# Kernel tuning notes

Hardware: AMD Instinct MI355X
Metric: run time of the kernel (lower is better)

Reference implementation:

```python
import jax, jax.numpy as jnp
import numpy as np

N_NODES = 50000
N_EDGES = 800000
D_IN, D_HID, D_OUT = 128, 128, 64


def setup_inputs() -> dict:
    key = jax.random.key(0)
    ks = jax.random.split(key, 10)
    return {
        "x": jax.random.normal(ks[0], (N_NODES, D_IN), dtype=jnp.float32),
        "edge_row": jax.random.randint(ks[1], (N_EDGES,), 0, N_NODES, dtype=jnp.int32),
        "edge_col": jax.random.randint(ks[2], (N_EDGES,), 0, N_NODES, dtype=jnp.int32),
        "edge_val": jax.random.uniform(ks[3], (N_EDGES,), dtype=jnp.float32),
        "W1": jax.random.normal(ks[4], (D_IN, D_HID), dtype=jnp.float32) * (1.0 / np.sqrt(D_HID)),
        "b1": jax.random.normal(ks[5], (D_HID,), dtype=jnp.float32) * (1.0 / np.sqrt(D_HID)),
        "W2": jax.random.normal(ks[6], (D_HID, D_HID), dtype=jnp.float32) * (1.0 / np.sqrt(D_HID)),
        "b2": jax.random.normal(ks[7], (D_HID,), dtype=jnp.float32) * (1.0 / np.sqrt(D_HID)),
        "W3": jax.random.normal(ks[8], (D_HID, D_OUT), dtype=jnp.float32) * (1.0 / np.sqrt(D_OUT)),
        "b3": jax.random.normal(ks[9], (D_OUT,), dtype=jnp.float32) * (1.0 / np.sqrt(D_OUT)),
    }


def _gcn_layer(x, edge_row, edge_col, edge_val, W, b):
    # support = x @ W          : dense GEMM [N, d_out]
    support = x @ W
    # spmm(adj, support)[i] = sum_e with row[e]==i: val[e] * support[col[e]]
    gathered = support[edge_col] * edge_val[:, None]  # [E, d_out]
    agg = jax.ops.segment_sum(gathered, edge_row, num_segments=x.shape[0])
    return agg + b


def reference(x, edge_row, edge_col, edge_val, W1, b1, W2, b2, W3, b3):
    # Layer 1 + ReLU (dropout is identity in eval)
    h = jax.nn.relu(_gcn_layer(x, edge_row, edge_col, edge_val, W1, b1))
    # Layer 2 + ReLU
    h = jax.nn.relu(_gcn_layer(h, edge_row, edge_col, edge_val, W2, b2))
    # Layer 3 (no activation)
    return _gcn_layer(h, edge_row, edge_col, edge_val, W3, b3)
```

## Files before the change

kernel.cpp:

```cpp
#include <hip/hip_runtime.h>

#define N_NODES 50000
#define N_EDGES 800000
#define SCAN_TILE 2048
#define GEMM1_BLOCKS 768
#define FUSED_BLOCKS 512
#define FILL_BLOCKS ((N_EDGES + 255) / 256)

#define HB 64
#define EPB (N_EDGES / HB)
#define HGROUPS (EPB / 4)
#define HHALF (N_NODES / 2)
#define HHALF4 (HHALF / 4)

static_assert(N_NODES < 65536, "col must fit in 16 bits for packed CSR");
static_assert(N_EDGES % (4 * HB) == 0, "chunking must be exact");
static_assert(EPB < 65536, "packed u16 counts must not overflow");

typedef __attribute__((ext_vector_type(4))) float f32x4;
typedef __attribute__((ext_vector_type(8))) short bf16x8;

__device__ inline unsigned short f32_to_bf16(float f) {
    unsigned int u = __builtin_bit_cast(unsigned int, f);
    u += 0x7FFF + ((u >> 16) & 1);
    return (unsigned short)(u >> 16);
}
__device__ inline float bf16_to_f32(unsigned short h) {
    unsigned int u = ((unsigned int)h) << 16;
    return __builtin_bit_cast(float, u);
}

#define W128  (128 * 128)
#define W64   (128 * 64)

__global__ __launch_bounds__(256) void prep_hist(
    const int* __restrict__ erow, int* __restrict__ rank,
    int* __restrict__ bhist, int* __restrict__ done_,
    const float* __restrict__ W1, const float* __restrict__ W2,
    const float* __restrict__ W3,
    unsigned short* __restrict__ Wt1, unsigned short* __restrict__ Wt2,
    unsigned short* __restrict__ Wt3) {
    __shared__ int h[HHALF];
    const int tid = threadIdx.x;
    if (blockIdx.x < HB) {
        const int b = blockIdx.x;
        int4* h4 = reinterpret_cast<int4*>(h);
        for (int i = tid; i < HHALF4; i += 256) {
            int4 z = {0, 0, 0, 0};
            h4[i] = z;
        }
        __syncthreads();
        const int4* eg = reinterpret_cast<const int4*>(erow) + (size_t)b * HGROUPS;
        int4* rg = reinterpret_cast<int4*>(rank) + (size_t)b * HGROUPS;
        for (int g = tid; g < HGROUPS; g += 256) {
            int4 er = eg[g];
            int4 rk;
            int sh, o;
            sh = (er.x & 1) << 4;
            o = atomicAdd(&h[er.x >> 1], 1 << sh);
            rk.x = (o >> sh) & 0xFFFF;
            sh = (er.y & 1) << 4;
            o = atomicAdd(&h[er.y >> 1], 1 << sh);
            rk.y = (o >> sh) & 0xFFFF;
            sh = (er.z & 1) << 4;
            o = atomicAdd(&h[er.z >> 1], 1 << sh);
            rk.z = (o >> sh) & 0xFFFF;
            sh = (er.w & 1) << 4;
            o = atomicAdd(&h[er.w >> 1], 1 << sh);
            rk.w = (o >> sh) & 0xFFFF;
            rg[g] = rk;
        }
        __syncthreads();
        int4* dst = reinterpret_cast<int4*>(bhist + (size_t)b * HHALF);
        for (int i = tid; i < HHALF4; i += 256) dst[i] = h4[i];
        return;
    }
    long long r = (long long)(blockIdx.x - HB) * 256 + tid;
    if (r < W128) {
        int k = (int)r / 128, m = (int)r % 128;
        Wt1[m * 128 + k] = f32_to_bf16(W1[r]);
        return;
    }
    r -= W128;
    if (r < W128) {
        int k = (int)r / 128, m = (int)r % 128;
        Wt2[m * 128 + k] = f32_to_bf16(W2[r]);
        return;
    }
    r -= W128;
    if (r < W64) {
        int k = (int)r / 64, m = (int)r % 64;
        Wt3[m * 128 + k] = f32_to_bf16(W3[r]);
        return;
    }
    r -= W64;
    if (r == 0) *done_ = 0;
}

template <int NOUT>
__device__ __forceinline__ void mfma_phase(const unsigned short* Xs,
                                           const unsigned short* Ws,
                                           unsigned short* __restrict__ Yb,
                                           int block_row, int N) {
    constexpr int KP = 128 + 8;
    constexpr int NT = NOUT / 16;
    const int tid = threadIdx.x;
    const int wave = tid >> 6;
    const int lane = tid & 63;
    const int m = lane & 15;
    const int quad = lane >> 4;
    const int rowbase = wave * 16;

    f32x4 acc[NT];
#pragma unroll
    for (int t = 0; t < NT; ++t) acc[t] = (f32x4){0.f, 0.f, 0.f, 0.f};

#pragma unroll
    for (int kt = 0; kt < 4; ++kt) {
        bf16x8 a = *reinterpret_cast<const bf16x8*>(
            Xs + (rowbase + m) * KP + kt * 32 + quad * 8);
#pragma unroll
        for (int t = 0; t < NT; ++t) {
            bf16x8 b = *reinterpret_cast<const bf16x8*>(
                Ws + (t * 16 + m) * KP + kt * 32 + quad * 8);
            acc[t] = __builtin_amdgcn_mfma_f32_16x16x32_bf16(a, b, acc[t], 0, 0, 0);
        }
    }

#pragma unroll
    for (int t = 0; t < NT; ++t) {
#pragma unroll
        for (int r = 0; r < 4; ++r) {
            int grow = block_row + rowbase + quad * 4 + r;
            if (grow < N)
                Yb[(size_t)grow * NOUT + t * 16 + m] = f32_to_bf16(acc[t][r]);
        }
    }
}

__global__ __launch_bounds__(256) void gemm1(
    const float* __restrict__ x, const unsigned short* __restrict__ Wt,
    unsigned short* __restrict__ Yb, int N, int ntiles) {
    constexpr int KP = 128 + 8;
    __shared__ unsigned short Xs[64 * KP];
    __shared__ unsigned short Ws[128 * KP];
    const int tid = threadIdx.x;

    for (int idx = tid; idx < 128 * 16; idx += 256) {
        int r = idx >> 4, ch = idx & 15;
        uint4 v = *reinterpret_cast<const uint4*>(Wt + r * 128 + ch * 8);
        *reinterpret_cast<uint4*>(Ws + r * KP + ch * 8) = v;
    }

    for (int tile = blockIdx.x; tile < ntiles; tile += GEMM1_BLOCKS) {
        const int block_row = tile * 64;
        for (int idx = tid; idx < 64 * 16; idx += 256) {
            int r = idx >> 4, ch = idx & 15;
            int gr = block_row + r;
            if (gr >= N) gr = N - 1;
            const float4* xp =
                reinterpret_cast<const float4*>(x + (size_t)gr * 128 + ch * 8);
            float4 a = xp[0], b = xp[1];
            uint4 o;
            o.x = (unsigned int)f32_to_bf16(a.x) | ((unsigned int)f32_to_bf16(a.y) << 16);
            o.y = (unsigned int)f32_to_bf16(a.z) | ((unsigned int)f32_to_bf16(a.w) << 16);
            o.z = (unsigned int)f32_to_bf16(b.x) | ((unsigned int)f32_to_bf16(b.y) << 16);
            o.w = (unsigned int)f32_to_bf16(b.z) | ((unsigned int)f32_to_bf16(b.w) << 16);
            *reinterpret_cast<uint4*>(Xs + r * KP + ch * 8) = o;
        }
        __syncthreads();
        mfma_phase<128>(Xs, Ws, Yb, block_row, N);
        __syncthreads();
    }
}

__global__ void scan_fused(const int* __restrict__ bhist, int* __restrict__ tsum,
                           int* __restrict__ done, int* __restrict__ rptr,
                           int* __restrict__ bbase, int n, int ntiles) {
    __shared__ int sums[256];
    __shared__ int off_s;
    const int t = threadIdx.x;
    const int b = blockIdx.x;
    const int base = b * SCAN_TILE + t * 8;
    const int nidx = base >> 3;
    const int4* bh4 = reinterpret_cast<const int4*>(bhist);
    int v[8], pref[8];
#pragma unroll
    for (int i = 0; i < 8; ++i) v[i] = 0;
    if (base < n) {
        for (int hb = 0; hb < HB; ++hb) {
            int4 p = bh4[hb * HHALF4 + nidx];
            v[0] += p.x & 0xFFFF; v[1] += (int)((unsigned)p.x >> 16);
            v[2] += p.y & 0xFFFF; v[3] += (int)((unsigned)p.y >> 16);
            v[4] += p.z & 0xFFFF; v[5] += (int)((unsigned)p.z >> 16);
            v[6] += p.w & 0xFFFF; v[7] += (int)((unsigned)p.w >> 16);
        }
    }
    int s = 0;
#pragma unroll
    for (int i = 0; i < 8; ++i) s += v[i];
    sums[t] = s;
    __syncthreads();
    for (int off = 1; off < 256; off <<= 1) {
        int x = (t >= off) ? sums[t - off] : 0;
        __syncthreads();
        sums[t] += x;
        __syncthreads();
    }
    int run = sums[t] - s;
#pragma unroll
    for (int i = 0; i < 8; ++i) {
        pref[i] = run;
        run += v[i];
    }
    if (t == 255) {
        tsum[b] = run;
        __threadfence();
        atomicAdd(done, 1);
    }
    if (t == 0) {
        while (__hip_atomic_load(done, __ATOMIC_ACQUIRE, __HIP_MEMORY_SCOPE_AGENT) <
               ntiles) {
        }
        __threadfence();
        int off = 0;
        for (int i = 0; i < b; ++i) off += tsum[i];
        off_s = off;
        if (b == 0) {
            int tot = 0;
            for (int i = 0; i < ntiles; ++i) tot += tsum[i];
            rptr[n] = tot;
        }
    }
    __syncthreads();
    const int off = off_s;
    if (base < n) {
        int rn[8];
#pragma unroll
        for (int i = 0; i < 8; ++i) rn[i] = pref[i] + off;
        int4 r0 = {rn[0], rn[1], rn[2], rn[3]};
        int4 r1 = {rn[4], rn[5], rn[6], rn[7]};
        *reinterpret_cast<int4*>(rptr + base) = r0;
        *reinterpret_cast<int4*>(rptr + base + 4) = r1;
        for (int hb = 0; hb < HB; ++hb) {
            int4 p = bh4[hb * HHALF4 + nidx];
            int4 o0 = {rn[0], rn[1], rn[2], rn[3]};
            int4 o1 = {rn[4], rn[5], rn[6], rn[7]};
            int4* bb = reinterpret_cast<int4*>(bbase + (size_t)hb * N_NODES + base);
            bb[0] = o0;
            bb[1] = o1;
            rn[0] += p.x & 0xFFFF; rn[1] += (int)((unsigned)p.x >> 16);
            rn[2] += p.y & 0xFFFF; rn[3] += (int)((unsigned)p.y >> 16);
            rn[4] += p.z & 0xFFFF; rn[5] += (int)((unsigned)p.z >> 16);
            rn[6] += p.w & 0xFFFF; rn[7] += (int)((unsigned)p.w >> 16);
        }
    }
}

__global__ void fill_csr(const int* __restrict__ erow, const int* __restrict__ ecol,
                         const float* __restrict__ eval, const int* __restrict__ bbase,
                         const int* __restrict__ rank,
                         unsigned int* __restrict__ cpack) {
    int e = blockIdx.x * blockDim.x + threadIdx.x;
    if (e >= N_EDGES) return;
    int slot = bbase[(size_t)(e / EPB) * N_NODES + erow[e]] + rank[e];
    unsigned int p = (unsigned int)(ecol[e] & 0xFFFF) |
                     ((unsigned int)f32_to_bf16(eval[e]) << 16);
    cpack[slot] = p;
}

template <int NOUT>
__device__ __forceinline__ void mfma_phase512(const unsigned short* Xs,
                                              const unsigned short* Ws,
                                              unsigned short* __restrict__ Yb,
                                              int block_row, int N) {
    constexpr int KP = 128 + 8;
    constexpr int NT = NOUT / 16;
    constexpr int NTH = NT / 2;
    const int tid = threadIdx.x;
    const int wave = tid >> 6;
    const int lane = tid & 63;
    const int m = lane & 15;
    const int quad = lane >> 4;
    const int rowbase = (wave & 3) * 16;
    const int tbase = (wave >> 2) * NTH;

    f32x4 acc[NTH];
#pragma unroll
    for (int t = 0; t < NTH; ++t) acc[t] = (f32x4){0.f, 0.f, 0.f, 0.f};

#pragma unroll
    for (int kt = 0; kt < 4; ++kt) {
        bf16x8 a = *reinterpret_cast<const bf16x8*>(
            Xs + (rowbase + m) * KP + kt * 32 + quad * 8);
#pragma unroll
        for (int t = 0; t < NTH; ++t) {
            bf16x8 b = *reinterpret_cast<const bf16x8*>(
                Ws + ((tbase + t) * 16 + m) * KP + kt * 32 + quad * 8);
            acc[t] = __builtin_amdgcn_mfma_f32_16x16x32_bf16(a, b, acc[t], 0, 0, 0);
        }
    }

#pragma unroll
    for (int t = 0; t < NTH; ++t) {
#pragma unroll
        for (int r = 0; r < 4; ++r) {
            int grow = block_row + rowbase + quad * 4 + r;
            if (grow < N)
                Yb[(size_t)grow * NOUT + (tbase + t) * 16 + m] = f32_to_bf16(acc[t][r]);
        }
    }
}

template <int NOUT>
__global__ __launch_bounds__(512, 4) void gemm_fused_agg(
    const unsigned short* __restrict__ S,
    const int* __restrict__ rptr, const unsigned int* __restrict__ cpack,
    const float* __restrict__ bias,
    const unsigned short* __restrict__ Wt,
    unsigned short* __restrict__ Yb,
    int N, int ntiles) {
    constexpr int KP = 128 + 8;
    __shared__ unsigned short Xs[64 * KP];
    __shared__ unsigned short Ws[NOUT * KP];
    const int tid = threadIdx.x;
    const int group = tid >> 4;
    const int f8 = tid & 15;

    for (int idx = tid; idx < NOUT * 16; idx += 512) {
        int r = idx >> 4, ch = idx & 15;
        uint4 v = *reinterpret_cast<const uint4*>(Wt + r * 128 + ch * 8);
        *reinterpret_cast<uint4*>(Ws + r * KP + ch * 8) = v;
    }

    float bv[8];
#pragma unroll
    for (int i = 0; i < 8; ++i) bv[i] = bias[f8 * 8 + i];

    for (int tile = blockIdx.x; tile < ntiles; tile += gridDim.x) {
        const int block_row = tile * 64;
#pragma unroll
        for (int r4 = 0; r4 < 2; ++r4) {
            const int row = r4 * 32 + group;
            const int node = block_row + row;
            float acc[8];
#pragma unroll
            for (int i = 0; i < 8; ++i) acc[i] = bv[i];
            if (node < N) {
                const int beg = rptr[node];
                const int end = rptr[node + 1];
                int j = beg;
                for (; j + 8 <= end; j += 8) {
                    unsigned int p[8];
                    uint4 s[8];
#pragma unroll
                    for (int u = 0; u < 8; ++u) p[u] = cpack[j + u];
#pragma unroll
                    for (int u = 0; u < 8; ++u)
                        s[u] = *reinterpret_cast<const uint4*>(
                            S + (size_t)(p[u] & 0xFFFF) * 128 + f8 * 8);
#pragma unroll
                    for (int u = 0; u < 8; ++u) {
                        const float v = bf16_to_f32((unsigned short)(p[u] >> 16));
                        const unsigned short* sp =
                            reinterpret_cast<const unsigned short*>(&s[u]);
#pragma unroll
                        for (int i = 0; i < 8; ++i)
                            acc[i] = fmaf(v, bf16_to_f32(sp[i]), acc[i]);
                    }
                }
                if (j + 4 <= end) {
                    unsigned int p[4];
                    uint4 s[4];
#pragma unroll
                    for (int u = 0; u < 4; ++u) p[u] = cpack[j + u];
#pragma unroll
                    for (int u = 0; u < 4; ++u)
                        s[u] = *reinterpret_cast<const uint4*>(
                            S + (size_t)(p[u] & 0xFFFF) * 128 + f8 * 8);
#pragma unroll
                    for (int u = 0; u < 4; ++u) {
                        const float v = bf16_to_f32((unsigned short)(p[u] >> 16));
                        const unsigned short* sp =
                            reinterpret_cast<const unsigned short*>(&s[u]);
#pragma unroll
                        for (int i = 0; i < 8; ++i)
                            acc[i] = fmaf(v, bf16_to_f32(sp[i]), acc[i]);
                    }
                    j += 4;
                }
                if (j + 2 <= end) {
                    unsigned int p[2];
                    uint4 s[2];
#pragma unroll
                    for (int u = 0; u < 2; ++u) p[u] = cpack[j + u];
#pragma unroll
                    for (int u = 0; u < 2; ++u)
                        s[u] = *reinterpret_cast<const uint4*>(
                            S + (size_t)(p[u] & 0xFFFF) * 128 + f8 * 8);
#pragma unroll
                    for (int u = 0; u < 2; ++u) {
                        const float v = bf16_to_f32((unsigned short)(p[u] >> 16));
                        const unsigned short* sp =
                            reinterpret_cast<const unsigned short*>(&s[u]);
#pragma unroll
                        for (int i = 0; i < 8; ++i)
                            acc[i] = fmaf(v, bf16_to_f32(sp[i]), acc[i]);
                    }
                    j += 2;
                }
                if (j < end) {
                    unsigned int p = cpack[j];
                    uint4 s = *reinterpret_cast<const uint4*>(
                        S + (size_t)(p & 0xFFFF) * 128 + f8 * 8);
                    const float v = bf16_to_f32((unsigned short)(p >> 16));
                    const unsigned short* sp =
                        reinterpret_cast<const unsigned short*>(&s);
#pragma unroll
                    for (int i = 0; i < 8; ++i)
                        acc[i] = fmaf(v, bf16_to_f32(sp[i]), acc[i]);
                }
            }
            uint4 o;
            o.x = (unsigned int)f32_to_bf16(fmaxf(acc[0], 0.f)) |
                  ((unsigned int)f32_to_bf16(fmaxf(acc[1], 0.f)) << 16);
            o.y = (unsigned int)f32_to_bf16(fmaxf(acc[2], 0.f)) |
                  ((unsigned int)f32_to_bf16(fmaxf(acc[3], 0.f)) << 16);
            o.z = (unsigned int)f32_to_bf16(fmaxf(acc[4], 0.f)) |
                  ((unsigned int)f32_to_bf16(fmaxf(acc[5], 0.f)) << 16);
            o.w = (unsigned int)f32_to_bf16(fmaxf(acc[6], 0.f)) |
                  ((unsigned int)f32_to_bf16(fmaxf(acc[7], 0.f)) << 16);
            *reinterpret_cast<uint4*>(Xs + row * KP + f8 * 8) = o;
        }
        __syncthreads();
        mfma_phase512<NOUT>(Xs, Ws, Yb, block_row, N);
        __syncthreads();
    }
}

__global__ void aggregate_bf16_64(const unsigned short* __restrict__ S,
                                  const int* __restrict__ rptr,
                                  const unsigned int* __restrict__ cpack,
                                  const float* __restrict__ bias,
                                  float* __restrict__ out, int N) {
    const int node = blockIdx.x * (blockDim.x / 8) + threadIdx.x / 8;
    const int f8 = threadIdx.x & 7;
    if (node >= N) return;
    const int beg = rptr[node];
    const int end = rptr[node + 1];
    float acc[8];
#pragma unroll
    for (int i = 0; i < 8; ++i) acc[i] = bias[f8 * 8 + i];
    int j = beg;
    for (; j + 8 <= end; j += 8) {
        unsigned int p[8];
        uint4 s[8];
#pragma unroll
        for (int u = 0; u < 8; ++u) p[u] = cpack[j + u];
#pragma unroll
        for (int u = 0; u < 8; ++u)
            s[u] = *reinterpret_cast<const uint4*>(S + (size_t)(p[u] & 0xFFFF) * 64 + f8 * 8);
#pragma unroll
        for (int u = 0; u < 8; ++u) {
            const float v = bf16_to_f32((unsigned short)(p[u] >> 16));
            const unsigned short* sp = reinterpret_cast<const unsigned short*>(&s[u]);
#pragma unroll
            for (int i = 0; i < 8; ++i) acc[i] = fmaf(v, bf16_to_f32(sp[i]), acc[i]);
        }
    }
    if (j + 4 <= end) {
        unsigned int p[4];
        uint4 s[4];
#pragma unroll
        for (int u = 0; u < 4; ++u) p[u] = cpack[j + u];
#pragma unroll
        for (int u = 0; u < 4; ++u)
            s[u] = *reinterpret_cast<const uint4*>(S + (size_t)(p[u] & 0xFFFF) * 64 + f8 * 8);
#pragma unroll
        for (int u = 0; u < 4; ++u) {
            const float v = bf16_to_f32((unsigned short)(p[u] >> 16));
            const unsigned short* sp = reinterpret_cast<const unsigned short*>(&s[u]);
#pragma unroll
            for (int i = 0; i < 8; ++i) acc[i] = fmaf(v, bf16_to_f32(sp[i]), acc[i]);
        }
        j += 4;
    }
    if (j + 2 <= end) {
        unsigned int p[2];
        uint4 s[2];
#pragma unroll
        for (int u = 0; u < 2; ++u) p[u] = cpack[j + u];
#pragma unroll
        for (int u = 0; u < 2; ++u)
            s[u] = *reinterpret_cast<const uint4*>(S + (size_t)(p[u] & 0xFFFF) * 64 + f8 * 8);
#pragma unroll
        for (int u = 0; u < 2; ++u) {
            const float v = bf16_to_f32((unsigned short)(p[u] >> 16));
            const unsigned short* sp = reinterpret_cast<const unsigned short*>(&s[u]);
#pragma unroll
            for (int i = 0; i < 8; ++i) acc[i] = fmaf(v, bf16_to_f32(sp[i]), acc[i]);
        }
        j += 2;
    }
    if (j < end) {
        unsigned int p = cpack[j];
        uint4 s = *reinterpret_cast<const uint4*>(S + (size_t)(p & 0xFFFF) * 64 + f8 * 8);
        const float v = bf16_to_f32((unsigned short)(p >> 16));
        const unsigned short* sp = reinterpret_cast<const unsigned short*>(&s);
#pragma unroll
        for (int i = 0; i < 8; ++i) acc[i] = fmaf(v, bf16_to_f32(sp[i]), acc[i]);
    }
    float4 o0 = {acc[0], acc[1], acc[2], acc[3]};
    float4 o1 = {acc[4], acc[5], acc[6], acc[7]};
    float* op = out + (size_t)node * 64 + f8 * 8;
    *reinterpret_cast<float4*>(op) = o0;
    *reinterpret_cast<float4*>(op + 4) = o1;
}

extern "C" void kernel_launch(void* const* d_in, const int* in_sizes, int n_in,
                              void* d_out, int out_size, void* d_ws, size_t ws_size,
                              hipStream_t stream) {
    const float* x    = (const float*)d_in[0];
    const int*   erow = (const int*)d_in[1];
    const int*   ecol = (const int*)d_in[2];
    const float* eval = (const float*)d_in[3];
    const float* W1   = (const float*)d_in[4];
    const float* b1   = (const float*)d_in[5];
    const float* W2   = (const float*)d_in[6];
    const float* b2   = (const float*)d_in[7];
    const float* W3   = (const float*)d_in[8];
    const float* b3   = (const float*)d_in[9];
    float* out = (float*)d_out;

    const size_t nf = (size_t)N_NODES * 128;
    unsigned short* SA  = (unsigned short*)d_ws;
    unsigned short* SB  = SA + nf;
    unsigned short* Wt1 = SB + nf;
    unsigned short* Wt2 = Wt1 + 128 * 128;
    unsigned short* Wt3 = Wt2 + 128 * 128;
    int*   rank   = (int*)(Wt3 + 64 * 128);
    int*   bhist  = rank + N_EDGES;
    int*   bbase  = bhist + (size_t)HB * HHALF;
    int*   rptr   = bbase + (size_t)HB * N_NODES;
    unsigned int* cpack = (unsigned int*)(rptr + N_NODES + 1);
    int*   stsum  = (int*)(cpack + N_EDGES);
    int*   done   = stsum + 32;

    const int blk = 256;
    const int ntiles_g = (N_NODES + 63) / 64;
    const int agg_grid = (int)(((long long)N_NODES * 8 + blk - 1) / blk);
    const int ntiles = (N_NODES + SCAN_TILE - 1) / SCAN_TILE;

    {
        long long wtotal = (long long)W128 + W128 + W64 + 1;
        int wblocks = (int)((wtotal + blk - 1) / blk);
        prep_hist<<<HB + wblocks, blk, 0, stream>>>(
            erow, rank, bhist, done, W1, W2, W3, Wt1, Wt2, Wt3);
    }

    gemm1<<<GEMM1_BLOCKS, 256, 0, stream>>>(x, Wt1, SA, N_NODES, ntiles_g);

    scan_fused<<<ntiles, 256, 0, stream>>>(bhist, stsum, done, rptr, bbase,
                                           N_NODES, ntiles);

    fill_csr<<<FILL_BLOCKS, blk, 0, stream>>>(erow, ecol, eval, bbase, rank, cpack);

    gemm_fused_agg<128><<<FUSED_BLOCKS, 512, 0, stream>>>(
        SA, rptr, cpack, b1, Wt2, SB, N_NODES, ntiles_g);

    gemm_fused_agg<64><<<FUSED_BLOCKS, 512, 0, stream>>>(
        SB, rptr, cpack, b2, Wt3, SA, N_NODES, ntiles_g);

    aggregate_bf16_64<<<agg_grid, blk, 0, stream>>>(SA, rptr, cpack, b3, out, N_NODES);
}
```

Before: 236.3 us.

## Fuse CSR build into GEMM1 and scan kernels, pack histograms as bytes

The row histogram moves into the first GEMM launch as extra blocks, and the scan and CSR fill become one kernel separated by a grid-wide atomic barrier. The per-block histogram counts and edge ranks shrink from 16-bit to 8-bit packing. The weight transpose and bf16 conversion now happen inside each GEMM block instead of in a separate prep kernel. Together these cut the launch count and the histogram and rank traffic. The costs are that every GEMM block repeats the weight conversion, the spin barrier needs all 960 blocks resident at once, and 8-bit counts overflow if one node gets 256 or more edges within a single chunk of 12500.

```diff
diff --git a/kernel.cpp b/kernel.cpp
--- a/kernel.cpp
+++ b/kernel.cpp
@@ -5,17 +5,16 @@
 #define SCAN_TILE 2048
 #define GEMM1_BLOCKS 768
 #define FUSED_BLOCKS 512
-#define FILL_BLOCKS ((N_EDGES + 255) / 256)
 
 #define HB 64
 #define EPB (N_EDGES / HB)
 #define HGROUPS (EPB / 4)
-#define HHALF (N_NODES / 2)
-#define HHALF4 (HHALF / 4)
+#define HWORDS (N_NODES / 4)
+#define SCANFILL_BLOCKS 960
 
 static_assert(N_NODES < 65536, "col must fit in 16 bits for packed CSR");
 static_assert(N_EDGES % (4 * HB) == 0, "chunking must be exact");
-static_assert(EPB < 65536, "packed u16 counts must not overflow");
+static_assert(N_NODES % 8 == 0, "scan tiles assume x8");
 
 typedef __attribute__((ext_vector_type(4))) float f32x4;
 typedef __attribute__((ext_vector_type(8))) short bf16x8;
@@ -28,73 +27,6 @@
 __device__ inline float bf16_to_f32(unsigned short h) {
     unsigned int u = ((unsigned int)h) << 16;
     return __builtin_bit_cast(float, u);
-}
-
-#define W128  (128 * 128)
-#define W64   (128 * 64)
-
-__global__ __launch_bounds__(256) void prep_hist(
-    const int* __restrict__ erow, int* __restrict__ rank,
-    int* __restrict__ bhist, int* __restrict__ done_,
-    const float* __restrict__ W1, const float* __restrict__ W2,
-    const float* __restrict__ W3,
-    unsigned short* __restrict__ Wt1, unsigned short* __restrict__ Wt2,
-    unsigned short* __restrict__ Wt3) {
-    __shared__ int h[HHALF];
-    const int tid = threadIdx.x;
-    if (blockIdx.x < HB) {
-        const int b = blockIdx.x;
-        int4* h4 = reinterpret_cast<int4*>(h);
-        for (int i = tid; i < HHALF4; i += 256) {
-            int4 z = {0, 0, 0, 0};
-            h4[i] = z;
-        }
-        __syncthreads();
-        const int4* eg = reinterpret_cast<const int4*>(erow) + (size_t)b * HGROUPS;
-        int4* rg = reinterpret_cast<int4*>(rank) + (size_t)b * HGROUPS;
-        for (int g = tid; g < HGROUPS; g += 256) {
-            int4 er = eg[g];
-            int4 rk;
-            int sh, o;
-            sh = (er.x & 1) << 4;
-            o = atomicAdd(&h[er.x >> 1], 1 << sh);
-            rk.x = (o >> sh) & 0xFFFF;
-            sh = (er.y & 1) << 4;
-            o = atomicAdd(&h[er.y >> 1], 1 << sh);
-            rk.y = (o >> sh) & 0xFFFF;
-            sh = (er.z & 1) << 4;
-            o = atomicAdd(&h[er.z >> 1], 1 << sh);
-            rk.z = (o >> sh) & 0xFFFF;
-            sh = (er.w & 1) << 4;
-            o = atomicAdd(&h[er.w >> 1], 1 << sh);
-            rk.w = (o >> sh) & 0xFFFF;
-            rg[g] = rk;
-        }
-        __syncthreads();
-        int4* dst = reinterpret_cast<int4*>(bhist + (size_t)b * HHALF);
-        for (int i = tid; i < HHALF4; i += 256) dst[i] = h4[i];
-        return;
-    }
-    long long r = (long long)(blockIdx.x - HB) * 256 + tid;
-    if (r < W128) {
-        int k = (int)r / 128, m = (int)r % 128;
-        Wt1[m * 128 + k] = f32_to_bf16(W1[r]);
-        return;
-    }
-    r -= W128;
-    if (r < W128) {
-        int k = (int)r / 128, m = (int)r % 128;
-        Wt2[m * 128 + k] = f32_to_bf16(W2[r]);
-        return;
-    }
-    r -= W128;
-    if (r < W64) {
-        int k = (int)r / 64, m = (int)r % 64;
-        Wt3[m * 128 + k] = f32_to_bf16(W3[r]);
-        return;
-    }
-    r -= W64;
-    if (r == 0) *done_ = 0;
 }
 
 template <int NOUT>
@@ -138,21 +70,63 @@
     }
 }
 
-__global__ __launch_bounds__(256) void gemm1(
-    const float* __restrict__ x, const unsigned short* __restrict__ Wt,
-    unsigned short* __restrict__ Yb, int N, int ntiles) {
+__global__ __launch_bounds__(256) void mega1(
+    const float* __restrict__ x, const float* __restrict__ W1,
+    unsigned short* __restrict__ Yb, int N, int ntiles,
+    const int* __restrict__ erow, unsigned int* __restrict__ rank8,
+    unsigned int* __restrict__ bhist, int* __restrict__ done,
+    int* __restrict__ done2) {
     constexpr int KP = 128 + 8;
-    __shared__ unsigned short Xs[64 * KP];
-    __shared__ unsigned short Ws[128 * KP];
+    __shared__ __align__(16) unsigned char smem[52224];
     const int tid = threadIdx.x;
 
-    for (int idx = tid; idx < 128 * 16; idx += 256) {
-        int r = idx >> 4, ch = idx & 15;
-        uint4 v = *reinterpret_cast<const uint4*>(Wt + r * 128 + ch * 8);
-        *reinterpret_cast<uint4*>(Ws + r * KP + ch * 8) = v;
-    }
-
-    for (int tile = blockIdx.x; tile < ntiles; tile += GEMM1_BLOCKS) {
+    if (blockIdx.x < HB) {
+        const int b = blockIdx.x;
+        if (b == 0 && tid == 0) { *done = 0; *done2 = 0; }
+        unsigned int* h = reinterpret_cast<unsigned int*>(smem);
+        int4* h4 = reinterpret_cast<int4*>(h);
+        for (int i = tid; i < HWORDS / 4; i += 256) {
+            int4 z = {0, 0, 0, 0};
+            h4[i] = z;
+        }
+        __syncthreads();
+        const int4* eg = reinterpret_cast<const int4*>(erow) + (size_t)b * HGROUPS;
+        unsigned int* rg = rank8 + (size_t)b * HGROUPS;
+        for (int g = tid; g < HGROUPS; g += 256) {
+            int4 er = eg[g];
+            unsigned int rk;
+            int sh;
+            unsigned int o;
+            sh = (er.x & 3) << 3;
+            o = atomicAdd(&h[er.x >> 2], 1u << sh);
+            rk = (o >> sh) & 0xFFu;
+            sh = (er.y & 3) << 3;
+            o = atomicAdd(&h[er.y >> 2], 1u << sh);
+            rk |= ((o >> sh) & 0xFFu) << 8;
+            sh = (er.z & 3) << 3;
+            o = atomicAdd(&h[er.z >> 2], 1u << sh);
+            rk |= ((o >> sh) & 0xFFu) << 16;
+            sh = (er.w & 3) << 3;
+            o = atomicAdd(&h[er.w >> 2], 1u << sh);
+            rk |= ((o >> sh) & 0xFFu) << 24;
+            rg[g] = rk;
+        }
+        __syncthreads();
+        int4* dst = reinterpret_cast<int4*>(bhist + (size_t)b * HWORDS);
+        for (int i = tid; i < HWORDS / 4; i += 256) dst[i] = h4[i];
+        return;
+    }
+
+    const int gb = blockIdx.x - HB;
+    unsigned short* Xs = reinterpret_cast<unsigned short*>(smem);
+    unsigned short* Ws = reinterpret_cast<unsigned short*>(smem) + 64 * KP;
+
+    for (int idx = tid; idx < 128 * 128; idx += 256) {
+        int k = idx >> 7, m = idx & 127;
+        Ws[m * KP + k] = f32_to_bf16(W1[idx]);
+    }
+
+    for (int tile = gb; tile < ntiles; tile += GEMM1_BLOCKS) {
         const int block_row = tile * 64;
         for (int idx = tid; idx < 64 * 16; idx += 256) {
             int r = idx >> 4, ch = idx & 15;
@@ -174,99 +148,116 @@
     }
 }
 
-__global__ void scan_fused(const int* __restrict__ bhist, int* __restrict__ tsum,
-                           int* __restrict__ done, int* __restrict__ rptr,
-                           int* __restrict__ bbase, int n, int ntiles) {
+__global__ __launch_bounds__(256, 4) void scan_fill(
+    const unsigned int* __restrict__ bhist, int* __restrict__ tsum,
+    int* __restrict__ done, int* __restrict__ done2,
+    int* __restrict__ rptr, int* __restrict__ bbase,
+    const int* __restrict__ erow, const int* __restrict__ ecol,
+    const float* __restrict__ eval, const unsigned int* __restrict__ rank8,
+    unsigned int* __restrict__ cpack, int n, int ntiles) {
     __shared__ int sums[256];
     __shared__ int off_s;
     const int t = threadIdx.x;
     const int b = blockIdx.x;
-    const int base = b * SCAN_TILE + t * 8;
-    const int nidx = base >> 3;
-    const int4* bh4 = reinterpret_cast<const int4*>(bhist);
-    int v[8], pref[8];
-#pragma unroll
-    for (int i = 0; i < 8; ++i) v[i] = 0;
-    if (base < n) {
-        for (int hb = 0; hb < HB; ++hb) {
-            int4 p = bh4[hb * HHALF4 + nidx];
-            v[0] += p.x & 0xFFFF; v[1] += (int)((unsigned)p.x >> 16);
-            v[2] += p.y & 0xFFFF; v[3] += (int)((unsigned)p.y >> 16);
-            v[4] += p.z & 0xFFFF; v[5] += (int)((unsigned)p.z >> 16);
-            v[6] += p.w & 0xFFFF; v[7] += (int)((unsigned)p.w >> 16);
-        }
-    }
-    int s = 0;
-#pragma unroll
-    for (int i = 0; i < 8; ++i) s += v[i];
-    sums[t] = s;
+
+    if (b < ntiles) {
+        const int base = b * SCAN_TILE + t * 8;
+        const int widx2 = base >> 3;
+        const uint2* bh2 = reinterpret_cast<const uint2*>(bhist);
+        int v[8], pref[8];
+#pragma unroll
+        for (int i = 0; i < 8; ++i) v[i] = 0;
+        if (base < n) {
+            for (int hb = 0; hb < HB; ++hb) {
+                uint2 p = bh2[hb * (HWORDS / 2) + widx2];
+                v[0] += p.x & 0xFF; v[1] += (p.x >> 8) & 0xFF;
+                v[2] += (p.x >> 16) & 0xFF; v[3] += p.x >> 24;
+                v[4] += p.y & 0xFF; v[5] += (p.y >> 8) & 0xFF;
+                v[6] += (p.y >> 16) & 0xFF; v[7] += p.y >> 24;
+            }
+        }
+        int s = 0;
+#pragma unroll
+        for (int i = 0; i < 8; ++i) s += v[i];
+        sums[t] = s;
+        __syncthreads();
+        for (int off = 1; off < 256; off <<= 1) {
+            int x = (t >= off) ? sums[t - off] : 0;
+            __syncthreads();
+            sums[t] += x;
+            __syncthreads();
+        }
+        int run = sums[t] - s;
+#pragma unroll
+        for (int i = 0; i < 8; ++i) {
+            pref[i] = run;
+            run += v[i];
+        }
+        if (t == 255) {
+            tsum[b] = run;
+            __threadfence();
+            atomicAdd(done, 1);
+        }
+        if (t == 0) {
+            while (__hip_atomic_load(done, __ATOMIC_ACQUIRE,
+                                     __HIP_MEMORY_SCOPE_AGENT) < ntiles) {
+            }
+            __threadfence();
+            int off = 0;
+            for (int i = 0; i < b; ++i) off += tsum[i];
+            off_s = off;
+            if (b == 0) {
+                int tot = 0;
+                for (int i = 0; i < ntiles; ++i) tot += tsum[i];
+                rptr[n] = tot;
+            }
+        }
+        __syncthreads();
+        const int off = off_s;
+        if (base < n) {
+            int rn[8];
+#pragma unroll
+            for (int i = 0; i < 8; ++i) rn[i] = pref[i] + off;
+            int4 r0 = {rn[0], rn[1], rn[2], rn[3]};
+            int4 r1 = {rn[4], rn[5], rn[6], rn[7]};
+            *reinterpret_cast<int4*>(rptr + base) = r0;
+            *reinterpret_cast<int4*>(rptr + base + 4) = r1;
+            for (int hb = 0; hb < HB; ++hb) {
+                int4 o0 = {rn[0], rn[1], rn[2], rn[3]};
+                int4 o1 = {rn[4], rn[5], rn[6], rn[7]};
+                int4* bb = reinterpret_cast<int4*>(
+                    bbase + (size_t)hb * N_NODES + base);
+                bb[0] = o0;
+                bb[1] = o1;
+                uint2 p = bh2[hb * (HWORDS / 2) + widx2];
+                rn[0] += p.x & 0xFF; rn[1] += (p.x >> 8) & 0xFF;
+                rn[2] += (p.x >> 16) & 0xFF; rn[3] += p.x >> 24;
+                rn[4] += p.y & 0xFF; rn[5] += (p.y >> 8) & 0xFF;
+                rn[6] += (p.y >> 16) & 0xFF; rn[7] += p.y >> 24;
+            }
+        }
+        __syncthreads();
+        if (t == 0) {
+            __threadfence();
+            atomicAdd(done2, 1);
+        }
+    }
+
+    if (t == 0) {
+        while (__hip_atomic_load(done2, __ATOMIC_ACQUIRE,
+                                 __HIP_MEMORY_SCOPE_AGENT) < ntiles) {
+        }
+    }
     __syncthreads();
-    for (int off = 1; off < 256; off <<= 1) {
-        int x = (t >= off) ? sums[t - off] : 0;
-        __syncthreads();
-        sums[t] += x;
-        __syncthreads();
-    }
-    int run = sums[t] - s;
-#pragma unroll
-    for (int i = 0; i < 8; ++i) {
-        pref[i] = run;
-        run += v[i];
-    }
-    if (t == 255) {
-        tsum[b] = run;
-        __threadfence();
-        atomicAdd(done, 1);
-    }
-    if (t == 0) {
-        while (__hip_atomic_load(done, __ATOMIC_ACQUIRE, __HIP_MEMORY_SCOPE_AGENT) <
-               ntiles) {
-        }
-        __threadfence();
-        int off = 0;
-        for (int i = 0; i < b; ++i) off += tsum[i];
-        off_s = off;
-        if (b == 0) {
-            int tot = 0;
-            for (int i = 0; i < ntiles; ++i) tot += tsum[i];
-            rptr[n] = tot;
-        }
-    }
-    __syncthreads();
-    const int off = off_s;
-    if (base < n) {
-        int rn[8];
-#pragma unroll
-        for (int i = 0; i < 8; ++i) rn[i] = pref[i] + off;
-        int4 r0 = {rn[0], rn[1], rn[2], rn[3]};
-        int4 r1 = {rn[4], rn[5], rn[6], rn[7]};
-        *reinterpret_cast<int4*>(rptr + base) = r0;
-        *reinterpret_cast<int4*>(rptr + base + 4) = r1;
-        for (int hb = 0; hb < HB; ++hb) {
-            int4 p = bh4[hb * HHALF4 + nidx];
-            int4 o0 = {rn[0], rn[1], rn[2], rn[3]};
-            int4 o1 = {rn[4], rn[5], rn[6], rn[7]};
-            int4* bb = reinterpret_cast<int4*>(bbase + (size_t)hb * N_NODES + base);
-            bb[0] = o0;
-            bb[1] = o1;
-            rn[0] += p.x & 0xFFFF; rn[1] += (int)((unsigned)p.x >> 16);
-            rn[2] += p.y & 0xFFFF; rn[3] += (int)((unsigned)p.y >> 16);
-            rn[4] += p.z & 0xFFFF; rn[5] += (int)((unsigned)p.z >> 16);
-            rn[6] += p.w & 0xFFFF; rn[7] += (int)((unsigned)p.w >> 16);
-        }
-    }
-}
-
-__global__ void fill_csr(const int* __restrict__ erow, const int* __restrict__ ecol,
-                         const float* __restrict__ eval, const int* __restrict__ bbase,
-                         const int* __restrict__ rank,
-                         unsigned int* __restrict__ cpack) {
-    int e = blockIdx.x * blockDim.x + threadIdx.x;
-    if (e >= N_EDGES) return;
-    int slot = bbase[(size_t)(e / EPB) * N_NODES + erow[e]] + rank[e];
-    unsigned int p = (unsigned int)(ecol[e] & 0xFFFF) |
-                     ((unsigned int)f32_to_bf16(eval[e]) << 16);
-    cpack[slot] = p;
+    __threadfence();
+    const unsigned char* r8 = reinterpret_cast<const unsigned char*>(rank8);
+    for (int e = b * 256 + t; e < N_EDGES; e += SCANFILL_BLOCKS * 256) {
+        int row = erow[e];
+        int slot = bbase[(size_t)(e / EPB) * N_NODES + row] + r8[e];
+        unsigned int pk = (unsigned int)(ecol[e] & 0xFFFF) |
+                          ((unsigned int)f32_to_bf16(eval[e]) << 16);
+        cpack[slot] = pk;
+    }
 }
 
 template <int NOUT>
@@ -317,7 +308,7 @@
     const unsigned short* __restrict__ S,
     const int* __restrict__ rptr, const unsigned int* __restrict__ cpack,
     const float* __restrict__ bias,
-    const unsigned short* __restrict__ Wt,
+    const float* __restrict__ W,
     unsigned short* __restrict__ Yb,
     int N, int ntiles) {
     constexpr int KP = 128 + 8;
@@ -327,10 +318,9 @@
     const int group = tid >> 4;
     const int f8 = tid & 15;
 
-    for (int idx = tid; idx < NOUT * 16; idx += 512) {
-        int r = idx >> 4, ch = idx & 15;
-        uint4 v = *reinterpret_cast<const uint4*>(Wt + r * 128 + ch * 8);
-        *reinterpret_cast<uint4*>(Ws + r * KP + ch * 8) = v;
+    for (int idx = tid; idx < 128 * NOUT; idx += 512) {
+        int k = idx / NOUT, m = idx % NOUT;
+        Ws[m * KP + k] = f32_to_bf16(W[idx]);
     }
 
     float bv[8];
@@ -533,43 +523,34 @@
     float* out = (float*)d_out;
 
     const size_t nf = (size_t)N_NODES * 128;
-    unsigned short* SA  = (unsigned short*)d_ws;
-    unsigned short* SB  = SA + nf;
-    unsigned short* Wt1 = SB + nf;
-    unsigned short* Wt2 = Wt1 + 128 * 128;
-    unsigned short* Wt3 = Wt2 + 128 * 128;
-    int*   rank   = (int*)(Wt3 + 64 * 128);
-    int*   bhist  = rank + N_EDGES;
-    int*   bbase  = bhist + (size_t)HB * HHALF;
+    unsigned short* SA   = (unsigned short*)d_ws;
+    unsigned short* SB   = SA + nf;
+    unsigned int*  rank8 = (unsigned int*)(SB + nf);
+    unsigned int*  bhist = rank8 + N_EDGES / 4;
+    int*   bbase  = (int*)(bhist + (size_t)HB * HWORDS);
     int*   rptr   = bbase + (size_t)HB * N_NODES;
     unsigned int* cpack = (unsigned int*)(rptr + N_NODES + 1);
     int*   stsum  = (int*)(cpack + N_EDGES);
-    int*   done   = stsum + 32;
+    int*   done   = stsum + 64;
+    int*   done2  = stsum + 80;
 
     const int blk = 256;
     const int ntiles_g = (N_NODES + 63) / 64;
     const int agg_grid = (int)(((long long)N_NODES * 8 + blk - 1) / blk);
     const int ntiles = (N_NODES + SCAN_TILE - 1) / SCAN_TILE;
 
-    {
-        long long wtotal = (long long)W128 + W128 + W64 + 1;
-        int wblocks = (int)((wtotal + blk - 1) / blk);
-        prep_hist<<<HB + wblocks, blk, 0, stream>>>(
-            erow, rank, bhist, done, W1, W2, W3, Wt1, Wt2, Wt3);
-    }
-
-    gemm1<<<GEMM1_BLOCKS, 256, 0, stream>>>(x, Wt1, SA, N_NODES, ntiles_g);
-
-    scan_fused<<<ntiles, 256, 0, stream>>>(bhist, stsum, done, rptr, bbase,
-                                           N_NODES, ntiles);
-
-    fill_csr<<<FILL_BLOCKS, blk, 0, stream>>>(erow, ecol, eval, bbase, rank, cpack);
+    mega1<<<HB + GEMM1_BLOCKS, blk, 0, stream>>>(
+        x, W1, SA, N_NODES, ntiles_g, erow, rank8, bhist, done, done2);
+
+    scan_fill<<<SCANFILL_BLOCKS, blk, 0, stream>>>(
+        bhist, stsum, done, done2, rptr, bbase, erow, ecol, eval, rank8,
+        cpack, N_NODES, ntiles);
 
     gemm_fused_agg<128><<<FUSED_BLOCKS, 512, 0, stream>>>(
-        SA, rptr, cpack, b1, Wt2, SB, N_NODES, ntiles_g);
+        SA, rptr, cpack, b1, W2, SB, N_NODES, ntiles_g);
 
     gemm_fused_agg<64><<<FUSED_BLOCKS, 512, 0, stream>>>(
-        SB, rptr, cpack, b2, Wt3, SA, N_NODES, ntiles_g);
+        SB, rptr, cpack, b2, W3, SA, N_NODES, ntiles_g);
 
     aggregate_bf16_64<<<agg_grid, blk, 0, stream>>>(SA, rptr, cpack, b3, out, N_NODES);
 }
```

Result: slower. 643.2 us (+172.2%).
